# Kernel tuning notes

Measured on AMD Instinct MI355X. Metric: run time of the kernel, lower is better.

Reference implementation:

```python
import jax, jax.numpy as jnp
import numpy as np

N, E = 50000, 800000
F_IN, F_H, H, F_OUT = 128, 16, 8, 64
NEG_SLOPE = 0.2
LN_EPS = 1e-5


def setup_inputs() -> dict:
    key = jax.random.key(0)
    ks = jax.random.split(key, 8)
    g = lambda k, shp, fan: (jax.random.normal(k, shp, jnp.float32) / np.sqrt(fan).astype(np.float32))
    return {
        "x": jax.random.normal(ks[0], (N, F_IN), jnp.float32),
        "edge_index": jax.random.randint(ks[1], (2, E), 0, N, jnp.int32),
        "Wl1": g(ks[2], (F_IN, H * F_H), F_IN),
        "Wr1": g(ks[3], (F_IN, H * F_H), F_IN),
        "att1": g(ks[4], (H, F_H), F_H),
        "bias1": jnp.zeros((H * F_H,), jnp.float32),
        "g1": jnp.ones((H * F_H,), jnp.float32),
        "b1": jnp.zeros((H * F_H,), jnp.float32),
        "Wl2": g(ks[5], (H * F_H, F_OUT), H * F_H),
        "Wr2": g(ks[6], (H * F_H, F_OUT), H * F_H),
        "att2": g(ks[7], (1, F_OUT), F_OUT),
        "bias2": jnp.zeros((F_OUT,), jnp.float32),
        "g2": jnp.ones((F_OUT,), jnp.float32),
        "b2": jnp.zeros((F_OUT,), jnp.float32),
    }


def gatv2_conv(x, edge_index, Wl, Wr, att, bias, concat):
    """PyG GATv2Conv (eval mode, dropout inactive).
    message m_e = leaky_relu(xl[src] + xr[dst]); alpha = softmax_dst(<m_e, att>);
    out_i = sum_{e: dst=i} alpha_e * xl[src_e]. Concat or mean over heads, + bias.
    """
    n = x.shape[0]
    h, c = att.shape
    src, dst = edge_index[0], edge_index[1]
    xl = (x @ Wl).reshape(n, h, c)  # source transform (lin_l)
    xr = (x @ Wr).reshape(n, h, c)  # target transform (lin_r)
    e = jax.nn.leaky_relu(xl[src] + xr[dst], NEG_SLOPE)  # [E,h,c]
    a = jnp.einsum("ehc,hc->eh", e, att)  # [E,h]
    # segment softmax over destination node
    m = jax.ops.segment_max(a, dst, num_segments=n)  # [n,h]
    m = jnp.where(jnp.isfinite(m), m, 0.0)  # isolated nodes -> -inf guard
    ea = jnp.exp(a - m[dst])
    s = jax.ops.segment_sum(ea, dst, num_segments=n)
    alpha = ea / (s[dst] + 1e-16)  # [E,h]
    out = jax.ops.segment_sum(xl[src] * alpha[..., None], dst, num_segments=n)  # [n,h,c]
    out = out.reshape(n, h * c) if concat else out.mean(axis=1)
    return out + bias


def layer_norm(x, gamma, beta):
    mu = x.mean(-1, keepdims=True)
    var = ((x - mu) ** 2).mean(-1, keepdims=True)
    return (x - mu) * jax.lax.rsqrt(var + LN_EPS) * gamma + beta


def reference(x, edge_index, Wl1, Wr1, att1, bias1, g1, b1,
              Wl2, Wr2, att2, bias2, g2, b2):
    h1 = gatv2_conv(x, edge_index, Wl1, Wr1, att1, bias1, concat=True)
    h1 = jax.nn.elu(layer_norm(h1, g1, b1))
    h2 = gatv2_conv(h1, edge_index, Wl2, Wr2, att2, bias2, concat=False)
    return layer_norm(h2, g2, b2)
```

## Files before the change

### kernel.cpp

```cpp
#include <hip/hip_runtime.h>
#include <hip/hip_bf16.h>
#include <math.h>

typedef short s16x8 __attribute__((ext_vector_type(8)));
typedef float f32x4 __attribute__((ext_vector_type(4)));
typedef float f32x2 __attribute__((ext_vector_type(2)));

__device__ __forceinline__ float bflo(unsigned u) { return __uint_as_float(u << 16); }
__device__ __forceinline__ float bfhi(unsigned u) { return __uint_as_float(u & 0xffff0000u); }
__device__ __forceinline__ unsigned short f2bf(float f) {
    __hip_bfloat16 h = __float2bfloat16(f);
    return __builtin_bit_cast(unsigned short, h);
}
__device__ __forceinline__ f32x4 mfma_bf16(s16x8 a, s16x8 b, f32x4 c) {
    asm("v_mfma_f32_16x16x32_bf16 %0, %1, %2, %0" : "+v"(c) : "v"(a), "v"(b));
    return c;
}
__device__ __forceinline__ f32x2 unpk2(unsigned u) { return (f32x2){bflo(u), bfhi(u)}; }
__device__ __forceinline__ f32x2 plrelu(f32x2 x) {
    return __builtin_elementwise_max(x, x * 0.2f);
}

__global__ void degree_rank_kernel(const int* __restrict__ dst, int* __restrict__ deg,
                                   int* __restrict__ rank, int E) {
    int e = blockIdx.x * blockDim.x + threadIdx.x;
    if (e < E) rank[e] = atomicAdd(&deg[dst[e]], 1);
}

__global__ __launch_bounds__(1024) void scan_part_kernel(const int* __restrict__ deg,
                                                         int* __restrict__ off,
                                                         int* __restrict__ bsum, int n) {
    __shared__ int wsum[16];
    int t = threadIdx.x, lane = t & 63, w = t >> 6;
    int i = blockIdx.x * 4096 + t * 4;
    int4 v = make_int4(0, 0, 0, 0);
    if (i + 3 < n) v = *reinterpret_cast<const int4*>(&deg[i]);
    else {
        if (i < n) v.x = deg[i];
        if (i + 1 < n) v.y = deg[i + 1];
        if (i + 2 < n) v.z = deg[i + 2];
    }
    int tsum = v.x + v.y + v.z + v.w;
    int x = tsum;
    #pragma unroll
    for (int d = 1; d < 64; d <<= 1) { int y = __shfl_up(x, d); if (lane >= d) x += y; }
    if (lane == 63) wsum[w] = x;
    __syncthreads();
    if (t < 16) {
        int y = wsum[t];
        #pragma unroll
        for (int d = 1; d < 16; d <<= 1) { int z = __shfl_up(y, d); if (t >= d) y += z; }
        wsum[t] = y;
    }
    __syncthreads();
    int excl = ((w == 0) ? 0 : wsum[w - 1]) + (x - tsum);
    if (i < n) off[i] = excl;
    if (i + 1 < n) off[i + 1] = excl + v.x;
    if (i + 2 < n) off[i + 2] = excl + v.x + v.y;
    if (i + 3 < n) off[i + 3] = excl + v.x + v.y + v.z;
    if (t == 0) bsum[blockIdx.x] = 0;
    __syncthreads();
    if (t == 1023) bsum[blockIdx.x] = wsum[15];
}

__global__ __launch_bounds__(64) void scan_tops_kernel(const int* __restrict__ bsum,
                                                       int* __restrict__ tops,
                                                       int* __restrict__ off,
                                                       int nblk, int n) {
    int t = threadIdx.x;
    int v = (t < nblk) ? bsum[t] : 0;
    int x = v;
    #pragma unroll
    for (int d = 1; d < 64; d <<= 1) { int y = __shfl_up(x, d); if (t >= d) x += y; }
    if (t < nblk) tops[t] = x - v;
    if (t == 63) off[n] = x;
}

__global__ __launch_bounds__(1024) void scan_add_kernel(int* __restrict__ off,
                                                        const int* __restrict__ tops, int n) {
    int b = blockIdx.x;
    int base = tops[b];
    int i = b * 4096 + threadIdx.x * 4;
    if (i + 3 < n) {
        int4 v = *reinterpret_cast<const int4*>(&off[i]);
        v.x += base; v.y += base; v.z += base; v.w += base;
        *reinterpret_cast<int4*>(&off[i]) = v;
    } else {
        if (i < n) off[i] += base;
        if (i + 1 < n) off[i + 1] += base;
        if (i + 2 < n) off[i + 2] += base;
    }
}

__global__ void scatter_kernel(const int* __restrict__ src, const int* __restrict__ dst,
                               const int* __restrict__ off, const int* __restrict__ rank,
                               int* __restrict__ ssrc, int E) {
    int e = blockIdx.x * blockDim.x + threadIdx.x;
    if (e < E) {
        int d = dst[e];
        ssrc[off[d] + rank[e]] = src[e];
    }
}

__global__ void wt_prep_kernel(const float* __restrict__ Wl1, const float* __restrict__ Wr1,
                               const float* __restrict__ Wl2, const float* __restrict__ Wr2,
                               unsigned short* __restrict__ Wt1, unsigned short* __restrict__ Wt2) {
    int idx = blockIdx.x * 256 + threadIdx.x;
    if (idx < 256 * 128) {
        int n = idx >> 7, k = idx & 127;
        float v = (n < 128) ? Wl1[k * 128 + n] : Wr1[k * 128 + (n - 128)];
        Wt1[idx] = f2bf(v);
    } else if (idx < 256 * 128 + 128 * 128) {
        int j = idx - 256 * 128;
        int n = j >> 7, k = j & 127;
        float v = (n < 64) ? Wl2[k * 64 + n] : Wr2[k * 64 + (n - 64)];
        Wt2[j] = f2bf(v);
    }
}

template <int NOUT, bool AFP32>
__global__ __launch_bounds__(256) void mfma_gemm_kernel(
    const void* __restrict__ A, const unsigned short* __restrict__ Wt,
    unsigned short* __restrict__ Cl, unsigned short* __restrict__ Cr, int nrows) {
    constexpr int HALF = NOUT / 2;
    constexpr int CT = NOUT / 64;
    __shared__ unsigned short As[64 * 128];
    int t = threadIdx.x, lane = t & 63, wave = t >> 6;
    int row_base = blockIdx.x * 64;
    int rows_here = nrows - row_base;
    #pragma unroll
    for (int it = 0; it < 4; ++it) {
        int q = it * 256 + t;
        int r = q >> 4, c8 = q & 15;
        int su = r * 16 + (c8 ^ (r & 7));
        s16x8 v = {0, 0, 0, 0, 0, 0, 0, 0};
        if (r < rows_here) {
            if (AFP32) {
                const float4* g = reinterpret_cast<const float4*>(
                    (const float*)A + ((size_t)(row_base + r)) * 128 + c8 * 8);
                float4 v0 = g[0], v1 = g[1];
                union { s16x8 s; unsigned short u[8]; } pk;
                pk.u[0] = f2bf(v0.x); pk.u[1] = f2bf(v0.y);
                pk.u[2] = f2bf(v0.z); pk.u[3] = f2bf(v0.w);
                pk.u[4] = f2bf(v1.x); pk.u[5] = f2bf(v1.y);
                pk.u[6] = f2bf(v1.z); pk.u[7] = f2bf(v1.w);
                v = pk.s;
            } else {
                v = *reinterpret_cast<const s16x8*>(
                    (const unsigned short*)A + ((size_t)(row_base + r)) * 128 + c8 * 8);
            }
        }
        reinterpret_cast<s16x8*>(As)[su] = v;
    }
    __syncthreads();
    int m16 = lane & 15, kg = lane >> 4;
    int colw = wave * (NOUT / 4);
    s16x8 bfr[CT][4];
    const s16x8* Wt16 = reinterpret_cast<const s16x8*>(Wt);
    #pragma unroll
    for (int ct = 0; ct < CT; ++ct)
        #pragma unroll
        for (int ks = 0; ks < 4; ++ks)
            bfr[ct][ks] = Wt16[(size_t)(colw + ct * 16 + m16) * 16 + ks * 4 + kg];
    f32x4 acc[4][CT];
    #pragma unroll
    for (int rt = 0; rt < 4; ++rt)
        #pragma unroll
        for (int ct = 0; ct < CT; ++ct) acc[rt][ct] = (f32x4){0.f, 0.f, 0.f, 0.f};
    const s16x8* As16 = reinterpret_cast<const s16x8*>(As);
    int sw = m16 & 7;
    #pragma unroll
    for (int rt = 0; rt < 4; ++rt) {
        int abase = (rt * 16 + m16) * 16;
        #pragma unroll
        for (int ks = 0; ks < 4; ++ks) {
            s16x8 af = As16[abase + ((ks * 4 + kg) ^ sw)];
            #pragma unroll
            for (int ct = 0; ct < CT; ++ct)
                acc[rt][ct] = mfma_bf16(af, bfr[ct][ks], acc[rt][ct]);
        }
    }
    int rq = kg * 4;
    #pragma unroll
    for (int rt = 0; rt < 4; ++rt) {
        #pragma unroll
        for (int ct = 0; ct < CT; ++ct) {
            int n = colw + ct * 16 + m16;
            unsigned short* Cp = (n < HALF) ? (Cl + n) : (Cr + (n - HALF));
            int row0 = row_base + rt * 16 + rq;
            #pragma unroll
            for (int i = 0; i < 4; ++i) {
                int row = row0 + i;
                if (row < nrows) Cp[(size_t)row * HALF] = f2bf(acc[rt][ct][i]);
            }
        }
    }
}

__global__ __launch_bounds__(256) void gat1_kernel(
    const unsigned short* __restrict__ xl, const unsigned short* __restrict__ xr,
    const int* __restrict__ off, const int* __restrict__ ssrc,
    const float* __restrict__ att, const float* __restrict__ bias,
    const float* __restrict__ gamma, const float* __restrict__ beta,
    unsigned short* __restrict__ out, int n) {
    int lane = threadIdx.x & 63;
    int node = blockIdx.x * 4 + (threadIdx.x >> 6);
    if (node >= n) return;
    int h = lane >> 3;
    int i0 = h * 16 + ((lane & 7) << 1);
    f32x2 xrp = unpk2(*reinterpret_cast<const unsigned*>(xr + (size_t)node * 128 + i0));
    f32x2 atp = {att[i0], att[i0 + 1]};
    float s = 0.f;
    f32x2 ac = {0.f, 0.f};
    int beg = off[node], end = off[node + 1];
    int i = beg;
    for (; i + 4 <= end; i += 4) {
        int e0 = ssrc[i], e1 = ssrc[i + 1], e2 = ssrc[i + 2], e3 = ssrc[i + 3];
        unsigned u0 = *reinterpret_cast<const unsigned*>(xl + (size_t)e0 * 128 + i0);
        unsigned u1 = *reinterpret_cast<const unsigned*>(xl + (size_t)e1 * 128 + i0);
        unsigned u2 = *reinterpret_cast<const unsigned*>(xl + (size_t)e2 * 128 + i0);
        unsigned u3 = *reinterpret_cast<const unsigned*>(xl + (size_t)e3 * 128 + i0);
        f32x2 x0 = unpk2(u0), x1 = unpk2(u1), x2 = unpk2(u2), x3 = unpk2(u3);
        f32x2 q0 = plrelu(x0 + xrp) * atp;
        f32x2 q1 = plrelu(x1 + xrp) * atp;
        f32x2 q2 = plrelu(x2 + xrp) * atp;
        f32x2 q3 = plrelu(x3 + xrp) * atp;
        float p0 = q0.x + q0.y, p1 = q1.x + q1.y;
        float p2 = q2.x + q2.y, p3 = q3.x + q3.y;
        #pragma unroll
        for (int d = 1; d < 8; d <<= 1) {
            p0 += __shfl_xor(p0, d); p1 += __shfl_xor(p1, d);
            p2 += __shfl_xor(p2, d); p3 += __shfl_xor(p3, d);
        }
        float w0 = __expf(fminf(p0, 60.f));
        float w1 = __expf(fminf(p1, 60.f));
        float w2 = __expf(fminf(p2, 60.f));
        float w3 = __expf(fminf(p3, 60.f));
        s += (w0 + w1) + (w2 + w3);
        ac += w0 * x0 + w1 * x1;
        ac += w2 * x2 + w3 * x3;
    }
    for (; i < end; ++i) {
        int e = ssrc[i];
        f32x2 xv = unpk2(*reinterpret_cast<const unsigned*>(xl + (size_t)e * 128 + i0));
        f32x2 q = plrelu(xv + xrp) * atp;
        float p = q.x + q.y;
        #pragma unroll
        for (int d = 1; d < 8; d <<= 1) p += __shfl_xor(p, d);
        float w = __expf(fminf(p, 60.f));
        s += w; ac += w * xv;
    }
    float inv = 1.f / (s + 1e-16f);
    float o0 = ac.x * inv + bias[i0];
    float o1 = ac.y * inv + bias[i0 + 1];
    float tsum = o0 + o1;
    #pragma unroll
    for (int d = 1; d < 64; d <<= 1) tsum += __shfl_xor(tsum, d);
    float mu = tsum * (1.f / 128.f);
    float d0 = o0 - mu, d1 = o1 - mu;
    float vsum = d0 * d0 + d1 * d1;
    #pragma unroll
    for (int d = 1; d < 64; d <<= 1) vsum += __shfl_xor(vsum, d);
    float rs = rsqrtf(vsum * (1.f / 128.f) + 1e-5f);
    float y0 = d0 * rs * gamma[i0] + beta[i0];
    float y1 = d1 * rs * gamma[i0 + 1] + beta[i0 + 1];
    y0 = y0 > 0.f ? y0 : expm1f(y0);
    y1 = y1 > 0.f ? y1 : expm1f(y1);
    unsigned pk = (unsigned)f2bf(y0) | ((unsigned)f2bf(y1) << 16);
    *reinterpret_cast<unsigned*>(out + (size_t)node * 128 + i0) = pk;
}

__global__ __launch_bounds__(256) void gat2_kernel(
    const unsigned short* __restrict__ xl, const unsigned short* __restrict__ xr,
    const int* __restrict__ off, const int* __restrict__ ssrc,
    const float* __restrict__ att, const float* __restrict__ bias,
    const float* __restrict__ gamma, const float* __restrict__ beta,
    float* __restrict__ out, int n) {
    int lane = threadIdx.x & 63;
    int node = blockIdx.x * 4 + (threadIdx.x >> 6);
    if (node >= n) return;
    int half = lane >> 5;
    int c2 = (lane & 31) << 1;
    f32x2 xrp = unpk2(*reinterpret_cast<const unsigned*>(xr + (size_t)node * 64 + c2));
    f32x2 atp = {att[c2], att[c2 + 1]};
    float s = 0.f;
    f32x2 ac = {0.f, 0.f};
    int beg = off[node], end = off[node + 1];
    int i = beg;
    for (; i + 4 <= end; i += 4) {
        int eA = ssrc[i + half], eB = ssrc[i + 2 + half];
        f32x2 xA = unpk2(*reinterpret_cast<const unsigned*>(xl + (size_t)eA * 64 + c2));
        f32x2 xB = unpk2(*reinterpret_cast<const unsigned*>(xl + (size_t)eB * 64 + c2));
        f32x2 qA = plrelu(xA + xrp) * atp;
        f32x2 qB = plrelu(xB + xrp) * atp;
        float pA = qA.x + qA.y, pB = qB.x + qB.y;
        #pragma unroll
        for (int d = 1; d < 32; d <<= 1) {
            pA += __shfl_xor(pA, d); pB += __shfl_xor(pB, d);
        }
        float wA = __expf(fminf(pA, 60.f));
        float wB = __expf(fminf(pB, 60.f));
        s += wA + wB;
        ac += wA * xA + wB * xB;
    }
    for (; i < end; i += 2) {
        int e = i + half;
        bool valid = e < end;
        int se = ssrc[valid ? e : i];
        f32x2 xv = unpk2(*reinterpret_cast<const unsigned*>(xl + (size_t)se * 64 + c2));
        f32x2 q = plrelu(xv + xrp) * atp;
        float p = q.x + q.y;
        #pragma unroll
        for (int d = 1; d < 32; d <<= 1) p += __shfl_xor(p, d);
        float w = valid ? __expf(fminf(p, 60.f)) : 0.f;
        s += w; ac += w * xv;
    }
    s += __shfl_xor(s, 32);
    f32x2 aco = {__shfl_xor(ac.x, 32), __shfl_xor(ac.y, 32)};
    ac += aco;
    float inv = 1.f / (s + 1e-16f);
    float o0 = ac.x * inv + bias[c2];
    float o1 = ac.y * inv + bias[c2 + 1];
    float tsum = o0 + o1;
    #pragma unroll
    for (int d = 1; d < 32; d <<= 1) tsum += __shfl_xor(tsum, d);
    float mu = tsum * (1.f / 64.f);
    float d0 = o0 - mu, d1 = o1 - mu;
    float vsum = d0 * d0 + d1 * d1;
    #pragma unroll
    for (int d = 1; d < 32; d <<= 1) vsum += __shfl_xor(vsum, d);
    float rs = rsqrtf(vsum * (1.f / 64.f) + 1e-5f);
    if (half == 0) {
        float y0 = d0 * rs * gamma[c2] + beta[c2];
        float y1 = d1 * rs * gamma[c2 + 1] + beta[c2 + 1];
        *reinterpret_cast<float2*>(out + (size_t)node * 64 + c2) = make_float2(y0, y1);
    }
}

extern "C" void kernel_launch(void* const* d_in, const int* in_sizes, int n_in,
                              void* d_out, int out_size, void* d_ws, size_t ws_size,
                              hipStream_t stream) {
    const float* x = (const float*)d_in[0];
    const int* ei = (const int*)d_in[1];
    const float* Wl1 = (const float*)d_in[2];
    const float* Wr1 = (const float*)d_in[3];
    const float* att1 = (const float*)d_in[4];
    const float* bias1 = (const float*)d_in[5];
    const float* g1 = (const float*)d_in[6];
    const float* b1 = (const float*)d_in[7];
    const float* Wl2 = (const float*)d_in[8];
    const float* Wr2 = (const float*)d_in[9];
    const float* att2 = (const float*)d_in[10];
    const float* bias2 = (const float*)d_in[11];
    const float* g2 = (const float*)d_in[12];
    const float* b2 = (const float*)d_in[13];
    float* out = (float*)d_out;

    const int N = in_sizes[0] / 128;
    const int E = in_sizes[1] / 2;
    const int* src = ei;
    const int* dstp = ei + E;

    char* p = (char*)d_ws;
    auto alloc = [&](size_t bytes) -> char* {
        char* r = p;
        p += (bytes + 255) & ~(size_t)255;
        return r;
    };
    int* deg = (int*)alloc((size_t)N * 4);
    int* rank = (int*)alloc((size_t)E * 4);
    int* off = (int*)alloc((size_t)(N + 1) * 4);
    int* ssrc = (int*)alloc((size_t)E * 4);
    int* bsum = (int*)alloc(64 * 4);
    int* tops = (int*)alloc(64 * 4);
    unsigned short* Wt1 = (unsigned short*)alloc(256 * 128 * 2);
    unsigned short* Wt2 = (unsigned short*)alloc(128 * 128 * 2);
    unsigned short* bufA = (unsigned short*)alloc((size_t)N * 128 * 2);
    unsigned short* bufB = (unsigned short*)alloc((size_t)N * 128 * 2);
    unsigned short* h1u = (unsigned short*)alloc((size_t)N * 128 * 2);

    const int nblk = (N + 4095) / 4096;

    hipMemsetAsync(deg, 0, (size_t)N * 4, stream);
    degree_rank_kernel<<<(E + 255) / 256, 256, 0, stream>>>(dstp, deg, rank, E);
    wt_prep_kernel<<<(256 * 128 + 128 * 128 + 255) / 256, 256, 0, stream>>>(
        Wl1, Wr1, Wl2, Wr2, Wt1, Wt2);
    scan_part_kernel<<<nblk, 1024, 0, stream>>>(deg, off, bsum, N);
    scan_tops_kernel<<<1, 64, 0, stream>>>(bsum, tops, off, nblk, N);
    scan_add_kernel<<<nblk, 1024, 0, stream>>>(off, tops, N);
    scatter_kernel<<<(E + 255) / 256, 256, 0, stream>>>(src, dstp, off, rank, ssrc, E);

    int gblocks = (N + 63) / 64;
    mfma_gemm_kernel<256, true><<<gblocks, 256, 0, stream>>>(x, Wt1, bufA, bufB, N);
    gat1_kernel<<<(N + 3) / 4, 256, 0, stream>>>(bufA, bufB, off, ssrc, att1, bias1, g1, b1, h1u, N);
    mfma_gemm_kernel<128, false><<<gblocks, 256, 0, stream>>>(h1u, Wt2, bufA, bufB, N);
    gat2_kernel<<<(N + 3) / 4, 256, 0, stream>>>(bufA, bufB, off, ssrc, att2, bias2, g2, b2, out, N);
}
```

Measured before the change: 275.5 us.

## Use DPP reductions, vectorized GEMM stores, and 4-edge-per-wave gat2 aggregation

Replaces the shuffle-based head-dot reductions with DPP row operations in gat1 and gat2, which avoids LDS-routed cross-lane traffic. The MFMA operands are swapped so each lane holds four consecutive output columns, allowing 8-byte vector stores instead of scalar 2-byte strided stores. gat2 is restructured so 16 lanes cover one edge with 4 features each, processing 4 edges per wave iteration. It also drops a redundant bsum zero write in the scan. The new gat2 layout adds an extra cross-group reduction at the end, and correctness depends on the DPP row_shr/bcast controls reducing the intended lanes.

```diff
diff --git a/kernel.cpp b/kernel.cpp
--- a/kernel.cpp
+++ b/kernel.cpp
@@ -19,6 +19,18 @@
 __device__ __forceinline__ f32x2 unpk2(unsigned u) { return (f32x2){bflo(u), bfhi(u)}; }
 __device__ __forceinline__ f32x2 plrelu(f32x2 x) {
     return __builtin_elementwise_max(x, x * 0.2f);
+}
+template <int CTRL>
+__device__ __forceinline__ float dpp_add(float v) {
+    int y = __builtin_amdgcn_update_dpp(0, __builtin_bit_cast(int, v), CTRL, 0xf, 0xf, true);
+    return v + __builtin_bit_cast(float, y);
+}
+__device__ __forceinline__ float red8(float p) {
+    p = dpp_add<0xB1>(p); p = dpp_add<0x4E>(p); return dpp_add<0x141>(p);
+}
+__device__ __forceinline__ float red16(float p) {
+    p = dpp_add<0xB1>(p); p = dpp_add<0x4E>(p);
+    p = dpp_add<0x141>(p); return dpp_add<0x140>(p);
 }
 
 __global__ void degree_rank_kernel(const int* __restrict__ dst, int* __restrict__ deg,
@@ -58,7 +70,6 @@
     if (i + 1 < n) off[i + 1] = excl + v.x;
     if (i + 2 < n) off[i + 2] = excl + v.x + v.y;
     if (i + 3 < n) off[i + 3] = excl + v.x + v.y + v.z;
-    if (t == 0) bsum[blockIdx.x] = 0;
     __syncthreads();
     if (t == 1023) bsum[blockIdx.x] = wsum[15];
 }
@@ -177,21 +188,23 @@
             s16x8 af = As16[abase + ((ks * 4 + kg) ^ sw)];
             #pragma unroll
             for (int ct = 0; ct < CT; ++ct)
-                acc[rt][ct] = mfma_bf16(af, bfr[ct][ks], acc[rt][ct]);
+                acc[rt][ct] = mfma_bf16(bfr[ct][ks], af, acc[rt][ct]);
         }
     }
-    int rq = kg * 4;
     #pragma unroll
     for (int rt = 0; rt < 4; ++rt) {
-        #pragma unroll
-        for (int ct = 0; ct < CT; ++ct) {
-            int n = colw + ct * 16 + m16;
-            unsigned short* Cp = (n < HALF) ? (Cl + n) : (Cr + (n - HALF));
-            int row0 = row_base + rt * 16 + rq;
+        int row = row_base + rt * 16 + m16;
+        if (row < nrows) {
             #pragma unroll
-            for (int i = 0; i < 4; ++i) {
-                int row = row0 + i;
-                if (row < nrows) Cp[(size_t)row * HALF] = f2bf(acc[rt][ct][i]);
+            for (int ct = 0; ct < CT; ++ct) {
+                int n0 = colw + ct * 16 + kg * 4;
+                unsigned short* Cp = (n0 < HALF) ? (Cl + n0) : (Cr + (n0 - HALF));
+                ushort4 w4;
+                w4.x = f2bf(acc[rt][ct][0]);
+                w4.y = f2bf(acc[rt][ct][1]);
+                w4.z = f2bf(acc[rt][ct][2]);
+                w4.w = f2bf(acc[rt][ct][3]);
+                *reinterpret_cast<ushort4*>(&Cp[(size_t)row * HALF]) = w4;
             }
         }
     }
@@ -227,11 +240,12 @@
         f32x2 q3 = plrelu(x3 + xrp) * atp;
         float p0 = q0.x + q0.y, p1 = q1.x + q1.y;
         float p2 = q2.x + q2.y, p3 = q3.x + q3.y;
-        #pragma unroll
-        for (int d = 1; d < 8; d <<= 1) {
-            p0 += __shfl_xor(p0, d); p1 += __shfl_xor(p1, d);
-            p2 += __shfl_xor(p2, d); p3 += __shfl_xor(p3, d);
-        }
+        p0 = dpp_add<0xB1>(p0); p1 = dpp_add<0xB1>(p1);
+        p2 = dpp_add<0xB1>(p2); p3 = dpp_add<0xB1>(p3);
+        p0 = dpp_add<0x4E>(p0); p1 = dpp_add<0x4E>(p1);
+        p2 = dpp_add<0x4E>(p2); p3 = dpp_add<0x4E>(p3);
+        p0 = dpp_add<0x141>(p0); p1 = dpp_add<0x141>(p1);
+        p2 = dpp_add<0x141>(p2); p3 = dpp_add<0x141>(p3);
         float w0 = __expf(fminf(p0, 60.f));
         float w1 = __expf(fminf(p1, 60.f));
         float w2 = __expf(fminf(p2, 60.f));
@@ -244,9 +258,7 @@
         int e = ssrc[i];
         f32x2 xv = unpk2(*reinterpret_cast<const unsigned*>(xl + (size_t)e * 128 + i0));
         f32x2 q = plrelu(xv + xrp) * atp;
-        float p = q.x + q.y;
-        #pragma unroll
-        for (int d = 1; d < 8; d <<= 1) p += __shfl_xor(p, d);
+        float p = red8(q.x + q.y);
         float w = __expf(fminf(p, 60.f));
         s += w; ac += w * xv;
     }
@@ -279,61 +291,57 @@
     int lane = threadIdx.x & 63;
     int node = blockIdx.x * 4 + (threadIdx.x >> 6);
     if (node >= n) return;
-    int half = lane >> 5;
-    int c2 = (lane & 31) << 1;
-    f32x2 xrp = unpk2(*reinterpret_cast<const unsigned*>(xr + (size_t)node * 64 + c2));
-    f32x2 atp = {att[c2], att[c2 + 1]};
+    int j2 = lane >> 4;
+    int q = lane & 15;
+    int fb = q * 4;
+    uint2 uxr = *reinterpret_cast<const uint2*>(xr + (size_t)node * 64 + fb);
+    f32x2 xr0 = unpk2(uxr.x), xr1 = unpk2(uxr.y);
+    float4 at = *reinterpret_cast<const float4*>(att + fb);
+    f32x2 at0 = {at.x, at.y}, at1 = {at.z, at.w};
     float s = 0.f;
-    f32x2 ac = {0.f, 0.f};
+    f32x2 ac0 = {0.f, 0.f}, ac1 = {0.f, 0.f};
     int beg = off[node], end = off[node + 1];
-    int i = beg;
-    for (; i + 4 <= end; i += 4) {
-        int eA = ssrc[i + half], eB = ssrc[i + 2 + half];
-        f32x2 xA = unpk2(*reinterpret_cast<const unsigned*>(xl + (size_t)eA * 64 + c2));
-        f32x2 xB = unpk2(*reinterpret_cast<const unsigned*>(xl + (size_t)eB * 64 + c2));
-        f32x2 qA = plrelu(xA + xrp) * atp;
-        f32x2 qB = plrelu(xB + xrp) * atp;
-        float pA = qA.x + qA.y, pB = qB.x + qB.y;
-        #pragma unroll
-        for (int d = 1; d < 32; d <<= 1) {
-            pA += __shfl_xor(pA, d); pB += __shfl_xor(pB, d);
-        }
-        float wA = __expf(fminf(pA, 60.f));
-        float wB = __expf(fminf(pB, 60.f));
-        s += wA + wB;
-        ac += wA * xA + wB * xB;
-    }
-    for (; i < end; i += 2) {
-        int e = i + half;
-        bool valid = e < end;
-        int se = ssrc[valid ? e : i];
-        f32x2 xv = unpk2(*reinterpret_cast<const unsigned*>(xl + (size_t)se * 64 + c2));
-        f32x2 q = plrelu(xv + xrp) * atp;
-        float p = q.x + q.y;
-        #pragma unroll
-        for (int d = 1; d < 32; d <<= 1) p += __shfl_xor(p, d);
+    for (int base = beg; base < end; base += 4) {
+        int idx = base + j2;
+        bool valid = idx < end;
+        int e = ssrc[valid ? idx : beg];
+        uint2 u = *reinterpret_cast<const uint2*>(xl + (size_t)e * 64 + fb);
+        f32x2 x0 = unpk2(u.x), x1 = unpk2(u.y);
+        f32x2 g0 = plrelu(x0 + xr0) * at0;
+        f32x2 g1 = plrelu(x1 + xr1) * at1;
+        f32x2 gs = g0 + g1;
+        float p = red16(gs.x + gs.y);
         float w = valid ? __expf(fminf(p, 60.f)) : 0.f;
-        s += w; ac += w * xv;
-    }
-    s += __shfl_xor(s, 32);
-    f32x2 aco = {__shfl_xor(ac.x, 32), __shfl_xor(ac.y, 32)};
-    ac += aco;
+        s += w;
+        ac0 += w * x0;
+        ac1 += w * x1;
+    }
+    #pragma unroll
+    for (int d = 16; d <= 32; d <<= 1) {
+        s += __shfl_xor(s, d);
+        ac0.x += __shfl_xor(ac0.x, d); ac0.y += __shfl_xor(ac0.y, d);
+        ac1.x += __shfl_xor(ac1.x, d); ac1.y += __shfl_xor(ac1.y, d);
+    }
     float inv = 1.f / (s + 1e-16f);
-    float o0 = ac.x * inv + bias[c2];
-    float o1 = ac.y * inv + bias[c2 + 1];
-    float tsum = o0 + o1;
-    #pragma unroll
-    for (int d = 1; d < 32; d <<= 1) tsum += __shfl_xor(tsum, d);
+    float4 bi = *reinterpret_cast<const float4*>(bias + fb);
+    float o0 = ac0.x * inv + bi.x;
+    float o1 = ac0.y * inv + bi.y;
+    float o2 = ac1.x * inv + bi.z;
+    float o3 = ac1.y * inv + bi.w;
+    float tsum = red16((o0 + o1) + (o2 + o3));
     float mu = tsum * (1.f / 64.f);
-    float d0 = o0 - mu, d1 = o1 - mu;
-    float vsum = d0 * d0 + d1 * d1;
-    #pragma unroll
-    for (int d = 1; d < 32; d <<= 1) vsum += __shfl_xor(vsum, d);
-    float rs = rsqrtf(vsum * (1.f / 64.f) + 1e-5f);
-    if (half == 0) {
-        float y0 = d0 * rs * gamma[c2] + beta[c2];
-        float y1 = d1 * rs * gamma[c2 + 1] + beta[c2 + 1];
-        *reinterpret_cast<float2*>(out + (size_t)node * 64 + c2) = make_float2(y0, y1);
+    float d0 = o0 - mu, d1 = o1 - mu, d2 = o2 - mu, d3 = o3 - mu;
+    float vs = red16((d0 * d0 + d1 * d1) + (d2 * d2 + d3 * d3));
+    float rs = rsqrtf(vs * (1.f / 64.f) + 1e-5f);
+    if (j2 == 0) {
+        float4 ga = *reinterpret_cast<const float4*>(gamma + fb);
+        float4 be = *reinterpret_cast<const float4*>(beta + fb);
+        float4 y;
+        y.x = d0 * rs * ga.x + be.x;
+        y.y = d1 * rs * ga.y + be.y;
+        y.z = d2 * rs * ga.z + be.z;
+        y.w = d3 * rs * ga.w + be.w;
+        *reinterpret_cast<float4*>(out + (size_t)node * 64 + fb) = y;
     }
 }
 
```

Result: faster. 268.1 us (-2.7%).
